# Performance work log

Hardware: AMD Instinct MI355X
Metric: run time of the kernel (lower is better)

## Reference

```python
import jax, jax.numpy as jnp
import numpy as np

B, S, D, H, R = 32, 8192, 256, 512, 256
CLIP = 3.0
WARMUP_ETA = 1.0
EML_BIAS = 0.0
LN_EPS = 1e-5


def setup_inputs() -> dict:
    key = jax.random.key(0)
    ks = jax.random.split(key, 12)
    def lin(k, fi, fo):
        return jax.random.normal(k, (fi, fo), jnp.float32) / np.sqrt(fi)
    return {
        "slot_states": jax.random.normal(ks[0], (B, S, D), jnp.float32),
        "slot_mask": jax.random.randint(ks[1], (B, S), 0, 2) > 0,
        "ln_gamma": jnp.ones((D,), jnp.float32),
        "ln_beta": jnp.zeros((D,), jnp.float32),
        "dw1": lin(ks[2], D, H), "db1": jnp.zeros((H,), jnp.float32),
        "dw2": lin(ks[3], H, 1), "db2": jnp.zeros((1,), jnp.float32),
        "rw1": lin(ks[4], D, H), "rb1": jnp.zeros((H,), jnp.float32),
        "rw2": lin(ks[5], H, 1), "rb2": jnp.zeros((1,), jnp.float32),
        "vw": lin(ks[6], D, R), "vb": jnp.zeros((R,), jnp.float32),
    }


def _layernorm(x, g, b):
    mu = jnp.mean(x, axis=-1, keepdims=True)
    var = jnp.mean(jnp.square(x - mu), axis=-1, keepdims=True)
    return (x - mu) * jax.lax.rsqrt(var + LN_EPS) * g + b


def _mlp(x, w1, b1, w2, b2):
    h = jax.nn.gelu(x @ w1 + b1, approximate=False)  # torch nn.GELU default = exact
    return h @ w2 + b2


def _masked_softmax(logits, mask):
    neg_inf = jnp.asarray(-jnp.inf, logits.dtype)
    w = jax.nn.softmax(jnp.where(mask, logits, neg_inf), axis=1)
    w = jnp.where(mask, w, 0.0)
    norm = jnp.sum(w, axis=1, keepdims=True)
    return jnp.where(norm > 0.0, w / jnp.maximum(norm, 1e-12), 0.0)


def reference(slot_states, slot_mask, ln_gamma, ln_beta, dw1, db1, dw2, db2, rw1, rb1, rw2, rb2, vw, vb):
    normalized = _layernorm(slot_states, ln_gamma, ln_beta)      # [B,S,D]
    drive = _mlp(normalized, dw1, db1, dw2, db2)                 # [B,S,1]
    resistance = _mlp(normalized, rw1, rb1, rw2, rb2)            # [B,S,1]
    res_pos = jax.nn.softplus(resistance)
    score = jnp.clip(drive - WARMUP_ETA * res_pos + EML_BIAS, -CLIP, CLIP)
    logits = jnp.squeeze(score, -1)                              # [B,S]
    weights = _masked_softmax(logits, slot_mask)                 # [B,S]
    values = normalized @ vw + vb                                # [B,S,R]
    representation = jnp.einsum("bs,bsr->br", weights, values)   # [B,R]
    top_weights, top_indices = jax.lax.top_k(weights, 3)
    return (representation, weights, top_indices, top_weights, logits)
```

## Files before the change

### kernel.cpp

```cpp
#include <hip/hip_runtime.h>
#include <math.h>

#define SB 32
#define SS 8192
#define SD 256
#define SH 512
#define CLIPV 3.0f

typedef __attribute__((ext_vector_type(8))) _Float16 f16x8;
typedef __attribute__((ext_vector_type(4))) float f32x4;

typedef const __attribute__((address_space(1))) unsigned int gu32_t;
typedef __attribute__((address_space(3))) unsigned int lu32_t;

__device__ __forceinline__ void split16(float v, _Float16& h, _Float16& l) {
    h = (_Float16)v;
    l = (_Float16)(v - (float)h);
}

__device__ __forceinline__ float4 ntload4(const float* p) {
    f32x4 t = __builtin_nontemporal_load((const f32x4*)p);
    return make_float4(t[0], t[1], t[2], t[3]);
}

__global__ __launch_bounds__(256) void k_prepw(
    const float* __restrict__ dw1, const float* __restrict__ rw1,
    _Float16* __restrict__ WTh, _Float16* __restrict__ WTl)
{
    const int c = blockIdx.x;
    const float* src = (c < SH) ? (dw1 + c) : (rw1 + (c - SH));
    const int k = threadIdx.x;
    const float v = src[(size_t)k * SH];
    _Float16 h, l;
    split16(v, h, l);
    WTh[(size_t)c * SD + k] = h;
    WTl[(size_t)c * SD + k] = l;
}

__global__ __launch_bounds__(256, 2) void k_logits(
    const float* __restrict__ x,
    const float* __restrict__ gamma, const float* __restrict__ beta,
    const _Float16* __restrict__ WTh, const _Float16* __restrict__ WTl,
    const float* __restrict__ db1, const float* __restrict__ dw2, const float* __restrict__ db2,
    const float* __restrict__ rb1, const float* __restrict__ rw2, const float* __restrict__ rb2,
    float* __restrict__ logits, float* __restrict__ murstd)
{
    __shared__ __align__(16) char LDS[65536];

    const int tid = threadIdx.x;
    const size_t row0 = (size_t)blockIdx.x * 128;
    char* AhB = LDS;
    char* AlB = LDS + 32768;

    const int w  = tid >> 6;
    const int l  = tid & 63;
    const int lr = l & 15, lk = l >> 4;
    const unsigned aRowByte = (unsigned)((w*16 + lr) * 512);
    const unsigned aSwz     = (unsigned)((lr & 7) << 4);

    f16x8 AH0[8], AL0[8], AH1[8], AL1[8];

#define STAGE_HALF(HALF, AHREG, ALREG)                                        \
    {                                                                         \
        const int r = (tid & 15) | ((tid >> 6) << 4);                         \
        const int q = (tid >> 4) & 3;                                         \
        const size_t row = row0 + (size_t)(HALF * 64 + r);                    \
        const float* xr = x + row * SD + q * 64;                              \
        float4 v[16];                                                         \
        float s = 0.f, sq = 0.f;                                              \
        _Pragma("unroll")                                                     \
        for (int i = 0; i < 16; ++i) {                                        \
            v[i] = ntload4(xr + i * 4);                                       \
            s  += v[i].x + v[i].y + v[i].z + v[i].w;                          \
            sq += v[i].x*v[i].x + v[i].y*v[i].y + v[i].z*v[i].z + v[i].w*v[i].w; \
        }                                                                     \
        s  += __shfl_xor(s, 16);  s  += __shfl_xor(s, 32);                    \
        sq += __shfl_xor(sq, 16); sq += __shfl_xor(sq, 32);                   \
        const float mu   = s * (1.0f / SD);                                   \
        const float var  = sq * (1.0f / SD) - mu * mu;                        \
        const float rstd = rsqrtf(var + 1e-5f);                               \
        if (q == 0) { murstd[2*row] = mu; murstd[2*row + 1] = rstd; }         \
        const float4* g4 = (const float4*)(gamma + q * 64);                   \
        const float4* b4 = (const float4*)(beta  + q * 64);                   \
        _Pragma("unroll")                                                     \
        for (int i = 0; i < 16; i += 2) {                                     \
            const float4 ga = g4[i], gb = g4[i+1];                            \
            const float4 ba = b4[i], bb = b4[i+1];                            \
            float xn[8];                                                      \
            xn[0] = (v[i].x   - mu) * rstd * ga.x + ba.x;                     \
            xn[1] = (v[i].y   - mu) * rstd * ga.y + ba.y;                     \
            xn[2] = (v[i].z   - mu) * rstd * ga.z + ba.z;                     \
            xn[3] = (v[i].w   - mu) * rstd * ga.w + ba.w;                     \
            xn[4] = (v[i+1].x - mu) * rstd * gb.x + bb.x;                     \
            xn[5] = (v[i+1].y - mu) * rstd * gb.y + bb.y;                     \
            xn[6] = (v[i+1].z - mu) * rstd * gb.z + bb.z;                     \
            xn[7] = (v[i+1].w - mu) * rstd * gb.w + bb.w;                     \
            f16x8 H, L;                                                       \
            _Pragma("unroll")                                                 \
            for (int j = 0; j < 8; ++j) {                                     \
                _Float16 hh, ll;                                              \
                split16(xn[j], hh, ll);                                       \
                H[j] = hh;                                                    \
                L[j] = ll;                                                    \
            }                                                                 \
            unsigned int off = (unsigned)(r * 512 + q * 128 + i * 8);         \
            off ^= (unsigned)((r & 7) << 4);                                  \
            *(f16x8*)(AhB + off) = H;                                         \
            *(f16x8*)(AlB + off) = L;                                         \
        }                                                                     \
    }                                                                         \
    __syncthreads();                                                          \
    _Pragma("unroll")                                                         \
    for (int k = 0; k < 8; ++k) {                                             \
        const unsigned off = (aRowByte + (unsigned)(lk*16 + k*64)) ^ aSwz;    \
        AHREG[k] = *(const f16x8*)(AhB + off);                                \
        ALREG[k] = *(const f16x8*)(AlB + off);                                \
    }                                                                         \
    __syncthreads();

    STAGE_HALF(0, AH0, AL0)
    STAGE_HALF(1, AH1, AL1)
#undef STAGE_HALF

    const int  sIsLo  = w >> 1;
    const int  sCc0   = (w & 1) * 8;
#define STAGE_B(T, D)                                                         \
    {                                                                         \
        const char* gsrc0 = (sIsLo ? (const char*)WTl : (const char*)WTh)     \
                            + (size_t)(T) * 16384;                            \
        char* lbase = LDS + (D) * 32768 + sIsLo * 16384;                      \
        _Pragma("unroll")                                                     \
        for (int c8 = 0; c8 < 8; ++c8) {                                      \
            const int cc = sCc0 + c8;                                         \
            const unsigned o    = (unsigned)(cc * 1024 + l * 16);             \
            const unsigned osrc = o ^ ((((o >> 9) & 7u)) << 4);               \
            __builtin_amdgcn_global_load_lds(                                 \
                (gu32_t*)(gsrc0 + osrc),                                      \
                (lu32_t*)(lbase + o), 16, 0, 0);                              \
        }                                                                     \
    }

    STAGE_B(0, 0)
    __syncthreads();

    float pd[2][4], pr[2][4];
    #pragma unroll
    for (int mi = 0; mi < 2; ++mi)
        #pragma unroll
        for (int i = 0; i < 4; ++i) { pd[mi][i] = 0.f; pr[mi][i] = 0.f; }

    #pragma unroll 1
    for (int n = 0; n < 32; ++n) {
        if (n < 31) STAGE_B(n + 1, (n + 1) & 1)

        const char* dB = LDS + (n & 1) * 32768;
        f32x4 acc[2][2];
        #pragma unroll
        for (int mi = 0; mi < 2; ++mi)
            #pragma unroll
            for (int ni = 0; ni < 2; ++ni) acc[mi][ni] = (f32x4){0.f,0.f,0.f,0.f};

        #pragma unroll
        for (int k = 0; k < 8; ++k) {
            f16x8 bh[2], bl[2];
            #pragma unroll
            for (int ni = 0; ni < 2; ++ni) {
                const unsigned u  = (unsigned)((ni*16 + lr) * 512 + k*64 + lk*16);
                const unsigned ra = u ^ aSwz;
                bh[ni] = *(const f16x8*)(dB + ra);
                bl[ni] = *(const f16x8*)(dB + 16384 + ra);
            }
            #pragma unroll
            for (int mi = 0; mi < 2; ++mi) {
                const f16x8 ah = (mi == 0) ? AH0[k] : AH1[k];
                const f16x8 al = (mi == 0) ? AL0[k] : AL1[k];
                #pragma unroll
                for (int ni = 0; ni < 2; ++ni) {
                    acc[mi][ni] = __builtin_amdgcn_mfma_f32_16x16x32_f16(al, bh[ni], acc[mi][ni], 0, 0, 0);
                    acc[mi][ni] = __builtin_amdgcn_mfma_f32_16x16x32_f16(ah, bl[ni], acc[mi][ni], 0, 0, 0);
                    acc[mi][ni] = __builtin_amdgcn_mfma_f32_16x16x32_f16(ah, bh[ni], acc[mi][ni], 0, 0, 0);
                }
            }
        }
        const bool  isD = (n < 16);
        const float* __restrict__ B1 = isD ? db1 : rb1;
        const float* __restrict__ W2 = isD ? dw2 : rw2;
        #pragma unroll
        for (int ni = 0; ni < 2; ++ni) {
            const int col = (n & 15)*32 + ni*16 + lr;
            const float b1v = B1[col];
            const float w2v = W2[col];
            #pragma unroll
            for (int mi = 0; mi < 2; ++mi)
                #pragma unroll
                for (int rg = 0; rg < 4; ++rg) {
                    const float h = acc[mi][ni][rg] + b1v;
                    const float g = 0.5f * h * (1.0f + erff(h * 0.70710678118654752f));
                    if (isD) pd[mi][rg] = fmaf(g, w2v, pd[mi][rg]);
                    else     pr[mi][rg] = fmaf(g, w2v, pr[mi][rg]);
                }
        }
        __syncthreads();
    }
#undef STAGE_B

    #pragma unroll
    for (int m = 1; m <= 8; m <<= 1) {
        #pragma unroll
        for (int mi = 0; mi < 2; ++mi)
            #pragma unroll
            for (int i = 0; i < 4; ++i) {
                pd[mi][i] += __shfl_xor(pd[mi][i], m);
                pr[mi][i] += __shfl_xor(pr[mi][i], m);
            }
    }
    if (lr == 0) {
        const float b2 = db2[0], r2 = rb2[0];
        #pragma unroll
        for (int mi = 0; mi < 2; ++mi)
            #pragma unroll
            for (int rg = 0; rg < 4; ++rg) {
                const int row = mi*64 + w*16 + lk*4 + rg;
                const float D = pd[mi][rg] + b2;
                const float R = pr[mi][rg] + r2;
                const float sp = fmaxf(R, 0.f) + log1pf(expf(-fabsf(R)));
                float s = D - sp;
                s = fminf(CLIPV, fmaxf(-CLIPV, s));
                logits[row0 + (size_t)row] = s;
            }
    }
}

__global__ __launch_bounds__(256) void k_softmax_topk(
    const float* __restrict__ logits, const int* __restrict__ mask,
    float* __restrict__ weights, float* __restrict__ ti, float* __restrict__ tw,
    float* __restrict__ flags)
{
    const int b = blockIdx.x, tid = threadIdx.x;
    const float* lg = logits + (size_t)b * SS;
    const int*   mk = mask   + (size_t)b * SS;
    float*       wt = weights + (size_t)b * SS;
    __shared__ float rv[4];
    __shared__ int   ri[4];
    __shared__ int   sCh[3];

    float mx = -INFINITY;
    for (int s = tid; s < SS; s += 256) if (mk[s]) mx = fmaxf(mx, lg[s]);
    #pragma unroll
    for (int off = 32; off; off >>= 1) mx = fmaxf(mx, __shfl_xor(mx, off));
    if ((tid & 63) == 0) rv[tid >> 6] = mx;
    __syncthreads();
    mx = fmaxf(fmaxf(rv[0], rv[1]), fmaxf(rv[2], rv[3]));
    __syncthreads();

    float sm = 0.f;
    for (int s = tid; s < SS; s += 256) if (mk[s]) sm += expf(lg[s] - mx);
    #pragma unroll
    for (int off = 32; off; off >>= 1) sm += __shfl_xor(sm, off);
    if ((tid & 63) == 0) rv[tid >> 6] = sm;
    __syncthreads();
    const float Z = rv[0] + rv[1] + rv[2] + rv[3];
    __syncthreads();
    const bool  any = (Z > 0.f) && (mx > -INFINITY);
    const float inv = any ? 1.0f / Z : 0.f;

    for (int s = tid; s < SS; s += 256) {
        const float w = (mk[s] && any) ? expf(lg[s] - mx) * inv : 0.f;
        wt[s] = w;
    }
    if (tid == 0) flags[b] = any ? 1.f : 0.f;
    __syncthreads();

    for (int t = 0; t < 3; ++t) {
        float bv = -1.f; int bi = 0;
        for (int s = tid; s < SS; s += 256) {
            bool ex = false;
            for (int u = 0; u < t; ++u) ex = ex || (s == sCh[u]);
            if (ex) continue;
            const float w = wt[s];
            if (w > bv || (w == bv && s < bi)) { bv = w; bi = s; }
        }
        #pragma unroll
        for (int off = 32; off; off >>= 1) {
            const float ov = __shfl_xor(bv, off);
            const int   oi = __shfl_xor(bi, off);
            if (ov > bv || (ov == bv && oi < bi)) { bv = ov; bi = oi; }
        }
        if ((tid & 63) == 0) { rv[tid >> 6] = bv; ri[tid >> 6] = bi; }
        __syncthreads();
        if (tid == 0) {
            for (int w2 = 1; w2 < 4; ++w2)
                if (rv[w2] > rv[0] || (rv[w2] == rv[0] && ri[w2] < ri[0])) { rv[0] = rv[w2]; ri[0] = ri[w2]; }
            sCh[t] = ri[0];
            ti[b*3 + t] = (float)ri[0];
            tw[b*3 + t] = rv[0];
        }
        __syncthreads();
    }
}

__global__ __launch_bounds__(256) void k_wsum(
    const float* __restrict__ x, const float* __restrict__ weights,
    const float* __restrict__ murstd,
    const float* __restrict__ gamma, const float* __restrict__ beta,
    float* __restrict__ partials)
{
    const int c = blockIdx.x;
    const int b = blockIdx.y;
    const int d = threadIdx.x;
    const float gg = gamma[d], bb = beta[d];
    float acc = 0.f;
    const size_t base = (size_t)b * SS + (size_t)c * 128;
    for (int s = 0; s < 128; ++s) {
        const size_t row = base + s;
        const float w = weights[row];
        if (w != 0.f) {
            const float mu = murstd[2*row], rs = murstd[2*row+1];
            const float xv = __builtin_nontemporal_load(&x[row * SD + d]);
            acc = fmaf(w, (xv - mu) * rs * gg + bb, acc);
        }
    }
    partials[((size_t)b * 64 + c) * SD + d] = acc;
}

__global__ __launch_bounds__(256) void k_final(
    const float* __restrict__ partials, const float* __restrict__ flags,
    const float* __restrict__ vw, const float* __restrict__ vb,
    float* __restrict__ rep)
{
    const int b = blockIdx.x;
    const int t = threadIdx.x;
    __shared__ float sv[SD];
    float a = 0.f;
    for (int c = 0; c < 64; ++c) a += partials[((size_t)b * 64 + c) * SD + t];
    sv[t] = a;
    __syncthreads();
    const float f = flags[b];
    float r = vb[t] * f;
    for (int dd = 0; dd < SD; ++dd) r = fmaf(sv[dd], vw[(size_t)dd * 256 + t], r);
    rep[(size_t)b * 256 + t] = r;
}

extern "C" void kernel_launch(void* const* d_in, const int* in_sizes, int n_in,
                              void* d_out, int out_size, void* d_ws, size_t ws_size,
                              hipStream_t stream)
{
    const float* x     = (const float*)d_in[0];
    const int*   mask  = (const int*)  d_in[1];
    const float* gamma = (const float*)d_in[2];
    const float* beta  = (const float*)d_in[3];
    const float* dw1   = (const float*)d_in[4];
    const float* db1   = (const float*)d_in[5];
    const float* dw2   = (const float*)d_in[6];
    const float* db2   = (const float*)d_in[7];
    const float* rw1   = (const float*)d_in[8];
    const float* rb1   = (const float*)d_in[9];
    const float* rw2   = (const float*)d_in[10];
    const float* rb2   = (const float*)d_in[11];
    const float* vw    = (const float*)d_in[12];
    const float* vb    = (const float*)d_in[13];

    float* out     = (float*)d_out;
    float* rep     = out;
    float* weights = out + 8192;
    float* ti      = out + 8192 + 262144;
    float* tw      = ti + 96;
    float* logits  = tw + 96;

    float* ws       = (float*)d_ws;
    float* murstd   = ws;
    float* partials = ws + 524288;
    float* flags    = ws + 1048576;
    _Float16* WTh   = (_Float16*)(ws + 1048608);
    _Float16* WTl   = WTh + 262144;

    hipLaunchKernelGGL(k_prepw, dim3(1024), dim3(256), 0, stream,
                       dw1, rw1, WTh, WTl);
    hipLaunchKernelGGL(k_logits, dim3(2048), dim3(256), 0, stream,
                       x, gamma, beta, WTh, WTl,
                       db1, dw2, db2, rb1, rw2, rb2,
                       logits, murstd);
    hipLaunchKernelGGL(k_softmax_topk, dim3(32), dim3(256), 0, stream,
                       logits, mask, weights, ti, tw, flags);
    hipLaunchKernelGGL(k_wsum, dim3(64, 32), dim3(256), 0, stream,
                       x, weights, murstd, gamma, beta, partials);
    hipLaunchKernelGGL(k_final, dim3(32), dim3(256), 0, stream,
                       partials, flags, vw, vb, rep);
}
```

Before: 710.5 us.

## Halve LDS footprint by staging A hi/lo in turns and narrowing B tiles

Cuts the logits kernel's shared memory from 64 KB to 32 KB. The A hi and lo halves now take turns in one LDS region, with the lo part held in registers meanwhile. The B weight tile per iteration shrinks from 32 to 16 hidden columns, so the loop runs 64 iterations instead of 32. The goal is to fit more blocks per CU so that memory latency is hidden better. The cost is extra barriers, twice as many loop iterations with their syncs, and less MFMA work per B load.

```diff
diff --git a/kernel.cpp b/kernel.cpp
--- a/kernel.cpp
+++ b/kernel.cpp
@@ -45,12 +45,10 @@
     const float* __restrict__ rb1, const float* __restrict__ rw2, const float* __restrict__ rb2,
     float* __restrict__ logits, float* __restrict__ murstd)
 {
-    __shared__ __align__(16) char LDS[65536];
+    __shared__ __align__(16) char LDS[32768];
 
     const int tid = threadIdx.x;
     const size_t row0 = (size_t)blockIdx.x * 128;
-    char* AhB = LDS;
-    char* AlB = LDS + 32768;
 
     const int w  = tid >> 6;
     const int l  = tid & 63;
@@ -62,81 +60,93 @@
 
 #define STAGE_HALF(HALF, AHREG, ALREG)                                        \
     {                                                                         \
+        f16x8 Lreg[8];                                                        \
         const int r = (tid & 15) | ((tid >> 6) << 4);                         \
         const int q = (tid >> 4) & 3;                                         \
-        const size_t row = row0 + (size_t)(HALF * 64 + r);                    \
-        const float* xr = x + row * SD + q * 64;                              \
-        float4 v[16];                                                         \
-        float s = 0.f, sq = 0.f;                                              \
+        {                                                                     \
+            const size_t row = row0 + (size_t)(HALF * 64 + r);                \
+            const float* xr = x + row * SD + q * 64;                          \
+            float4 v[16];                                                     \
+            float s = 0.f, sq = 0.f;                                          \
+            _Pragma("unroll")                                                 \
+            for (int i = 0; i < 16; ++i) {                                    \
+                v[i] = ntload4(xr + i * 4);                                   \
+                s  += v[i].x + v[i].y + v[i].z + v[i].w;                      \
+                sq += v[i].x*v[i].x + v[i].y*v[i].y + v[i].z*v[i].z + v[i].w*v[i].w; \
+            }                                                                 \
+            s  += __shfl_xor(s, 16);  s  += __shfl_xor(s, 32);                \
+            sq += __shfl_xor(sq, 16); sq += __shfl_xor(sq, 32);               \
+            const float mu   = s * (1.0f / SD);                               \
+            const float var  = sq * (1.0f / SD) - mu * mu;                    \
+            const float rstd = rsqrtf(var + 1e-5f);                           \
+            if (q == 0) { murstd[2*row] = mu; murstd[2*row + 1] = rstd; }     \
+            const float4* g4 = (const float4*)(gamma + q * 64);               \
+            const float4* b4 = (const float4*)(beta  + q * 64);               \
+            _Pragma("unroll")                                                 \
+            for (int i = 0; i < 16; i += 2) {                                 \
+                const float4 ga = g4[i], gb = g4[i+1];                        \
+                const float4 ba = b4[i], bb = b4[i+1];                        \
+                float xn[8];                                                  \
+                xn[0] = (v[i].x   - mu) * rstd * ga.x + ba.x;                 \
+                xn[1] = (v[i].y   - mu) * rstd * ga.y + ba.y;                 \
+                xn[2] = (v[i].z   - mu) * rstd * ga.z + ba.z;                 \
+                xn[3] = (v[i].w   - mu) * rstd * ga.w + ba.w;                 \
+                xn[4] = (v[i+1].x - mu) * rstd * gb.x + bb.x;                 \
+                xn[5] = (v[i+1].y - mu) * rstd * gb.y + bb.y;                 \
+                xn[6] = (v[i+1].z - mu) * rstd * gb.z + bb.z;                 \
+                xn[7] = (v[i+1].w - mu) * rstd * gb.w + bb.w;                 \
+                f16x8 H, L;                                                   \
+                _Pragma("unroll")                                             \
+                for (int j = 0; j < 8; ++j) {                                 \
+                    _Float16 hh, ll;                                          \
+                    split16(xn[j], hh, ll);                                   \
+                    H[j] = hh;                                                \
+                    L[j] = ll;                                                \
+                }                                                             \
+                unsigned int off = (unsigned)(r * 512 + q * 128 + i * 8);     \
+                off ^= (unsigned)((r & 7) << 4);                              \
+                *(f16x8*)(LDS + off) = H;                                     \
+                Lreg[i >> 1] = L;                                             \
+            }                                                                 \
+        }                                                                     \
+        __syncthreads();                                                      \
         _Pragma("unroll")                                                     \
-        for (int i = 0; i < 16; ++i) {                                        \
-            v[i] = ntload4(xr + i * 4);                                       \
-            s  += v[i].x + v[i].y + v[i].z + v[i].w;                          \
-            sq += v[i].x*v[i].x + v[i].y*v[i].y + v[i].z*v[i].z + v[i].w*v[i].w; \
+        for (int k = 0; k < 8; ++k)                                           \
+            AHREG[k] = *(const f16x8*)(LDS +                                  \
+                ((aRowByte + (unsigned)(lk*16 + k*64)) ^ aSwz));              \
+        __syncthreads();                                                      \
+        _Pragma("unroll")                                                     \
+        for (int ip = 0; ip < 8; ++ip) {                                      \
+            unsigned int off = (unsigned)(r * 512 + q * 128 + ip * 16);       \
+            off ^= (unsigned)((r & 7) << 4);                                  \
+            *(f16x8*)(LDS + off) = Lreg[ip];                                  \
         }                                                                     \
-        s  += __shfl_xor(s, 16);  s  += __shfl_xor(s, 32);                    \
-        sq += __shfl_xor(sq, 16); sq += __shfl_xor(sq, 32);                   \
-        const float mu   = s * (1.0f / SD);                                   \
-        const float var  = sq * (1.0f / SD) - mu * mu;                        \
-        const float rstd = rsqrtf(var + 1e-5f);                               \
-        if (q == 0) { murstd[2*row] = mu; murstd[2*row + 1] = rstd; }         \
-        const float4* g4 = (const float4*)(gamma + q * 64);                   \
-        const float4* b4 = (const float4*)(beta  + q * 64);                   \
+        __syncthreads();                                                      \
         _Pragma("unroll")                                                     \
-        for (int i = 0; i < 16; i += 2) {                                     \
-            const float4 ga = g4[i], gb = g4[i+1];                            \
-            const float4 ba = b4[i], bb = b4[i+1];                            \
-            float xn[8];                                                      \
-            xn[0] = (v[i].x   - mu) * rstd * ga.x + ba.x;                     \
-            xn[1] = (v[i].y   - mu) * rstd * ga.y + ba.y;                     \
-            xn[2] = (v[i].z   - mu) * rstd * ga.z + ba.z;                     \
-            xn[3] = (v[i].w   - mu) * rstd * ga.w + ba.w;                     \
-            xn[4] = (v[i+1].x - mu) * rstd * gb.x + bb.x;                     \
-            xn[5] = (v[i+1].y - mu) * rstd * gb.y + bb.y;                     \
-            xn[6] = (v[i+1].z - mu) * rstd * gb.z + bb.z;                     \
-            xn[7] = (v[i+1].w - mu) * rstd * gb.w + bb.w;                     \
-            f16x8 H, L;                                                       \
-            _Pragma("unroll")                                                 \
-            for (int j = 0; j < 8; ++j) {                                     \
-                _Float16 hh, ll;                                              \
-                split16(xn[j], hh, ll);                                       \
-                H[j] = hh;                                                    \
-                L[j] = ll;                                                    \
-            }                                                                 \
-            unsigned int off = (unsigned)(r * 512 + q * 128 + i * 8);         \
-            off ^= (unsigned)((r & 7) << 4);                                  \
-            *(f16x8*)(AhB + off) = H;                                         \
-            *(f16x8*)(AlB + off) = L;                                         \
-        }                                                                     \
-    }                                                                         \
-    __syncthreads();                                                          \
-    _Pragma("unroll")                                                         \
-    for (int k = 0; k < 8; ++k) {                                             \
-        const unsigned off = (aRowByte + (unsigned)(lk*16 + k*64)) ^ aSwz;    \
-        AHREG[k] = *(const f16x8*)(AhB + off);                                \
-        ALREG[k] = *(const f16x8*)(AlB + off);                                \
-    }                                                                         \
-    __syncthreads();
+        for (int k = 0; k < 8; ++k)                                           \
+            ALREG[k] = *(const f16x8*)(LDS +                                  \
+                ((aRowByte + (unsigned)(lk*16 + k*64)) ^ aSwz));              \
+        __syncthreads();                                                      \
+    }
 
     STAGE_HALF(0, AH0, AL0)
     STAGE_HALF(1, AH1, AL1)
 #undef STAGE_HALF
 
-    const int  sIsLo  = w >> 1;
-    const int  sCc0   = (w & 1) * 8;
 #define STAGE_B(T, D)                                                         \
     {                                                                         \
-        const char* gsrc0 = (sIsLo ? (const char*)WTl : (const char*)WTh)     \
-                            + (size_t)(T) * 16384;                            \
-        char* lbase = LDS + (D) * 32768 + sIsLo * 16384;                      \
+        const size_t tb = (size_t)(T) * 8192;                                 \
+        char* lb = LDS + (D) * 16384;                                         \
         _Pragma("unroll")                                                     \
-        for (int c8 = 0; c8 < 8; ++c8) {                                      \
-            const int cc = sCc0 + c8;                                         \
-            const unsigned o    = (unsigned)(cc * 1024 + l * 16);             \
-            const unsigned osrc = o ^ ((((o >> 9) & 7u)) << 4);               \
+        for (int rr = 0; rr < 2; ++rr) {                                      \
+            const unsigned o  = (unsigned)(rr * 4096 + tid * 16);             \
+            const unsigned os = o ^ ((((o >> 9) & 7u)) << 4);                 \
             __builtin_amdgcn_global_load_lds(                                 \
-                (gu32_t*)(gsrc0 + osrc),                                      \
-                (lu32_t*)(lbase + o), 16, 0, 0);                              \
+                (gu32_t*)((const char*)WTh + tb + os),                        \
+                (lu32_t*)(lb + o), 16, 0, 0);                                 \
+            __builtin_amdgcn_global_load_lds(                                 \
+                (gu32_t*)((const char*)WTl + tb + os),                        \
+                (lu32_t*)(lb + 8192 + o), 16, 0, 0);                          \
         }                                                                     \
     }
 
@@ -150,51 +160,41 @@
         for (int i = 0; i < 4; ++i) { pd[mi][i] = 0.f; pr[mi][i] = 0.f; }
 
     #pragma unroll 1
-    for (int n = 0; n < 32; ++n) {
-        if (n < 31) STAGE_B(n + 1, (n + 1) & 1)
-
-        const char* dB = LDS + (n & 1) * 32768;
-        f32x4 acc[2][2];
-        #pragma unroll
-        for (int mi = 0; mi < 2; ++mi)
-            #pragma unroll
-            for (int ni = 0; ni < 2; ++ni) acc[mi][ni] = (f32x4){0.f,0.f,0.f,0.f};
+    for (int n = 0; n < 64; ++n) {
+        if (n < 63) STAGE_B(n + 1, (n + 1) & 1)
+
+        const char* dB = LDS + (n & 1) * 16384;
+        f32x4 acc[2];
+        #pragma unroll
+        for (int mi = 0; mi < 2; ++mi) acc[mi] = (f32x4){0.f,0.f,0.f,0.f};
 
         #pragma unroll
         for (int k = 0; k < 8; ++k) {
-            f16x8 bh[2], bl[2];
-            #pragma unroll
-            for (int ni = 0; ni < 2; ++ni) {
-                const unsigned u  = (unsigned)((ni*16 + lr) * 512 + k*64 + lk*16);
-                const unsigned ra = u ^ aSwz;
-                bh[ni] = *(const f16x8*)(dB + ra);
-                bl[ni] = *(const f16x8*)(dB + 16384 + ra);
-            }
+            const unsigned u  = (unsigned)(lr * 512 + k*64 + lk*16);
+            const unsigned ra = u ^ aSwz;
+            const f16x8 bh = *(const f16x8*)(dB + ra);
+            const f16x8 bl = *(const f16x8*)(dB + 8192 + ra);
             #pragma unroll
             for (int mi = 0; mi < 2; ++mi) {
                 const f16x8 ah = (mi == 0) ? AH0[k] : AH1[k];
                 const f16x8 al = (mi == 0) ? AL0[k] : AL1[k];
-                #pragma unroll
-                for (int ni = 0; ni < 2; ++ni) {
-                    acc[mi][ni] = __builtin_amdgcn_mfma_f32_16x16x32_f16(al, bh[ni], acc[mi][ni], 0, 0, 0);
-                    acc[mi][ni] = __builtin_amdgcn_mfma_f32_16x16x32_f16(ah, bl[ni], acc[mi][ni], 0, 0, 0);
-                    acc[mi][ni] = __builtin_amdgcn_mfma_f32_16x16x32_f16(ah, bh[ni], acc[mi][ni], 0, 0, 0);
-                }
+                acc[mi] = __builtin_amdgcn_mfma_f32_16x16x32_f16(al, bh, acc[mi], 0, 0, 0);
+                acc[mi] = __builtin_amdgcn_mfma_f32_16x16x32_f16(ah, bl, acc[mi], 0, 0, 0);
+                acc[mi] = __builtin_amdgcn_mfma_f32_16x16x32_f16(ah, bh, acc[mi], 0, 0, 0);
             }
         }
-        const bool  isD = (n < 16);
+        const bool  isD = (n < 32);
         const float* __restrict__ B1 = isD ? db1 : rb1;
         const float* __restrict__ W2 = isD ? dw2 : rw2;
-        #pragma unroll
-        for (int ni = 0; ni < 2; ++ni) {
-            const int col = (n & 15)*32 + ni*16 + lr;
+        {
+            const int col = (n & 31)*16 + lr;
             const float b1v = B1[col];
             const float w2v = W2[col];
             #pragma unroll
             for (int mi = 0; mi < 2; ++mi)
                 #pragma unroll
                 for (int rg = 0; rg < 4; ++rg) {
-                    const float h = acc[mi][ni][rg] + b1v;
+                    const float h = acc[mi][rg] + b1v;
                     const float g = 0.5f * h * (1.0f + erff(h * 0.70710678118654752f));
                     if (isD) pd[mi][rg] = fmaf(g, w2v, pd[mi][rg]);
                     else     pr[mi][rg] = fmaf(g, w2v, pr[mi][rg]);
```

Result: slower. 737.0 us (+3.7%).
